# Kernel optimization log

Measured on AMD Instinct MI355X. Metric: run time of the kernel, lower is better.

Reference implementation:

```python
import jax, jax.numpy as jnp
import numpy as np

N_NODES = 100000
FIELD_DIM = 128
EMBED_DIM = 64
N_EDGES = 3200000
BATCH = 8192
NUM_FIELDS = 2


def setup_inputs() -> dict:
    key = jax.random.key(0)
    k1, k2, k3, k4 = jax.random.split(key, 4)
    features = jax.random.normal(k1, (N_NODES, FIELD_DIM), dtype=jnp.float32)
    edge_index = jax.random.randint(k2, (2, N_EDGES), 0, N_NODES, dtype=jnp.int32)
    # GCNConv linear weight (Glorot-ish scale) and bias
    W = jax.random.normal(k3, (FIELD_DIM, EMBED_DIM), dtype=jnp.float32) * (1.0 / np.sqrt(FIELD_DIM))
    bias = jnp.zeros((EMBED_DIM,), dtype=jnp.float32)
    x = jax.random.randint(k4, (BATCH, NUM_FIELDS), 0, N_NODES, dtype=jnp.int32)
    return {"features": features, "edge_index": edge_index, "W": W, "bias": bias, "x": x}


def reference(features, edge_index, W, bias, x):
    # GCNConv: out = D^{-1/2} (A + I) D^{-1/2} (X W) + b, then gather rows by x.
    n = features.shape[0]
    loop = jnp.arange(n, dtype=edge_index.dtype)
    src = jnp.concatenate([edge_index[0], loop])  # [E + N]
    dst = jnp.concatenate([edge_index[1], loop])  # [E + N]
    # degree (with self-loops) per destination node; >= 1 so rsqrt is safe
    deg = jax.ops.segment_sum(jnp.ones_like(dst, dtype=features.dtype), dst, num_segments=n)
    dinv = jax.lax.rsqrt(deg)
    norm = dinv[src] * dinv[dst]  # [E + N]
    h = features @ W  # [N, EMBED_DIM]
    msgs = h[src] * norm[:, None]  # gather + scale
    out = jax.ops.segment_sum(msgs, dst, num_segments=n) + bias  # [N, EMBED_DIM]
    return out[x]  # [BATCH, NUM_FIELDS, EMBED_DIM]
```

## Files before the change

### kernel.cpp

```cpp
#include <hip/hip_runtime.h>

#define N_NODES   100000
#define FIELD_DIM 128
#define EMBED_DIM 64
#define N_EDGES   3200000
#define NX        16384

#define NRANGE    4
#define RN        25000
#define RNH       12500
#define NSLICE    125
#define SLICE_E   (N_EDGES / NSLICE)
#define HISTB     (NRANGE * NSLICE)
#define SB_N      16384
#define EXB       (N_EDGES / 1024)
#define SEG       256

typedef short  bf16x8 __attribute__((ext_vector_type(8)));
typedef float  f32x4  __attribute__((ext_vector_type(4)));

__device__ __forceinline__ unsigned short f2bf(float x) {
    unsigned u = __float_as_uint(x);
    u += 0x7FFF + ((u >> 16) & 1);
    return (unsigned short)(u >> 16);
}
__device__ __forceinline__ float bf2f(unsigned short b) {
    return __uint_as_float(((unsigned)b) << 16);
}
__device__ __forceinline__ unsigned pk2(float lo, float hi) {
    return (unsigned)f2bf(lo) | ((unsigned)f2bf(hi) << 16);
}

__global__ void k_zero(float4* __restrict__ z4) {
    int i = blockIdx.x * blockDim.x + threadIdx.x;
    if (i < 784) z4[i] = make_float4(0.f, 0.f, 0.f, 0.f);
}

__global__ void k_init(const int* __restrict__ x, unsigned int* __restrict__ bits,
                       const float* __restrict__ W, unsigned short* __restrict__ Wt) {
    int b = blockIdx.x;
    if (b < 64) {
        int i = b * 256 + threadIdx.x;
        int v = x[i];
        atomicOr(&bits[v >> 5], 1u << (v & 31));
    } else {
        for (int i = threadIdx.x; i < FIELD_DIM * EMBED_DIM; i += 256) {
            int k = i >> 6, c = i & 63;
            Wt[c * FIELD_DIM + k] = f2bf(W[i]);
        }
    }
}

__global__ __launch_bounds__(256) void k_hist(const int* __restrict__ dst,
                                              unsigned int* __restrict__ partial32) {
    __shared__ unsigned int hist[RNH];
    int tid = threadIdx.x;
    int q = blockIdx.x & 3, s = blockIdx.x >> 2;
    for (int i = tid; i < RNH; i += 256) hist[i] = 0;
    __syncthreads();
    int lo = q * RN;
    const int4* dp = (const int4*)(dst + s * SLICE_E);
#pragma unroll
    for (int bt = 0; bt < 5; ++bt) {
        int4 d[5];
#pragma unroll
        for (int u = 0; u < 5; ++u) d[u] = dp[tid + 256 * (bt * 5 + u)];
#pragma unroll
        for (int u = 0; u < 5; ++u) {
            int a;
            a = d[u].x - lo; if ((unsigned)a < RN) atomicAdd(&hist[a >> 1], 1u << ((a & 1) << 4));
            a = d[u].y - lo; if ((unsigned)a < RN) atomicAdd(&hist[a >> 1], 1u << ((a & 1) << 4));
            a = d[u].z - lo; if ((unsigned)a < RN) atomicAdd(&hist[a >> 1], 1u << ((a & 1) << 4));
            a = d[u].w - lo; if ((unsigned)a < RN) atomicAdd(&hist[a >> 1], 1u << ((a & 1) << 4));
        }
    }
    __syncthreads();
    unsigned int* po = partial32 + (size_t)blockIdx.x * RNH;
    for (int i = tid; i < RNH; i += 256) po[i] = hist[i];
}

__global__ __launch_bounds__(256) void k_reduce(const unsigned int* __restrict__ partial32,
                                                const unsigned int* __restrict__ bits,
                                                int* __restrict__ cnt,
                                                float* __restrict__ dinv,
                                                int* __restrict__ nlist,
                                                int* __restrict__ inv,
                                                int* __restrict__ off,
                                                int* __restrict__ sbase_t,
                                                unsigned long long* __restrict__ counters) {
    __shared__ int wtot[4], wedge[4], ptot[4], pedge[4];
    __shared__ unsigned int baseN, baseE;
    int tid = threadIdx.x;
    int v = blockIdx.x * 256 + tid;
    bool inb = (v < N_NODES);
    int vc = inb ? v : (N_NODES - 1);
    int q = vc / RN, loc = vc - q * RN;
    int i2 = loc >> 1, sh = (loc & 1) << 4;
    const unsigned int* p = partial32 + (size_t)q * RNH + i2;
    int c = 0;
#pragma unroll
    for (int sb = 0; sb < 5; ++sb) {
        unsigned int vals[25];
#pragma unroll
        for (int s = 0; s < 25; ++s) vals[s] = p[(size_t)(sb * 25 + s) * (NRANGE * RNH)];
#pragma unroll
        for (int s = 0; s < 25; ++s) c += (int)((vals[s] >> sh) & 0xFFFFu);
    }
    if (inb) {
        cnt[v] = c;
        dinv[v] = rsqrtf((float)c + 1.0f);
    }
    bool fl = inb && ((bits[v >> 5] >> (v & 31)) & 1u);
    int lane = tid & 63;
    int w = tid >> 6;
    unsigned long long mask = __ballot(fl);
    int cc = fl ? c : 0;
    int incl = cc;
#pragma unroll
    for (int o = 1; o < 64; o <<= 1) {
        int t = __shfl_up(incl, o);
        if (lane >= o) incl += t;
    }
    if (lane == 63) { wtot[w] = __popcll(mask); wedge[w] = incl; }
    int myi = __popcll(mask & ((1ull << lane) - 1));
    int excl = incl - cc;
    __syncthreads();
    if (tid == 0) {
        int t0 = wtot[0], t1 = wtot[1], t2 = wtot[2], t3 = wtot[3];
        int e0 = wedge[0], e1 = wedge[1], e2 = wedge[2], e3 = wedge[3];
        ptot[0] = 0; ptot[1] = t0; ptot[2] = t0 + t1; ptot[3] = t0 + t1 + t2;
        pedge[0] = 0; pedge[1] = e0; pedge[2] = e0 + e1; pedge[3] = e0 + e1 + e2;
        int bt = t0 + t1 + t2 + t3;
        int be = e0 + e1 + e2 + e3;
        if (bt > 0) {
            unsigned long long add = ((unsigned long long)(unsigned)be << 32) |
                                     (unsigned long long)(unsigned)bt;
            unsigned long long old = atomicAdd(counters, add);
            baseN = (unsigned)(old & 0xFFFFFFFFull);
            baseE = (unsigned)(old >> 32);
        } else {
            baseN = 0; baseE = 0;
        }
    }
    __syncthreads();
    if (fl) {
        int ic = (int)baseN + ptot[w] + myi;
        int oc = (int)baseE + pedge[w] + excl;
        nlist[ic] = v;
        inv[v] = ic;
        off[v] = oc;
        int cum = 0;
#pragma unroll
        for (int sb = 0; sb < 5; ++sb) {
            unsigned int vals[25];
#pragma unroll
            for (int s = 0; s < 25; ++s) vals[s] = p[(size_t)(sb * 25 + s) * (NRANGE * RNH)];
#pragma unroll
            for (int s = 0; s < 25; ++s) {
                sbase_t[(size_t)(sb * 25 + s) * SB_N + ic] = oc + cum;
                cum += (int)((vals[s] >> sh) & 0xFFFFu);
            }
        }
    }
}

__global__ __launch_bounds__(256) void k_extract(const int* __restrict__ src,
                                                 const int* __restrict__ dst,
                                                 const unsigned int* __restrict__ bits,
                                                 const int* __restrict__ inv,
                                                 int2* __restrict__ pairs,
                                                 int* __restrict__ pcnt) {
    __shared__ int wsum[4];
    int b = blockIdx.x, tid = threadIdx.x;
    int lane = tid & 63, w = tid >> 6;
    const int4* dp = (const int4*)(dst + b * 1024);
    const int4* sp = (const int4*)(src + b * 1024);
    int4 d4 = dp[tid];
    int4 s4 = sp[tid];
    int dd[4] = {d4.x, d4.y, d4.z, d4.w};
    int ss[4] = {s4.x, s4.y, s4.z, s4.w};
    bool fl[4];
    int nf = 0;
#pragma unroll
    for (int u = 0; u < 4; ++u) {
        fl[u] = (bits[(unsigned)dd[u] >> 5] >> (dd[u] & 31)) & 1u;
        nf += fl[u] ? 1 : 0;
    }
    int incl = nf;
#pragma unroll
    for (int o = 1; o < 64; o <<= 1) {
        int t = __shfl_up(incl, o);
        if (lane >= o) incl += t;
    }
    if (lane == 63) wsum[w] = incl;
    __syncthreads();
    int wbase = 0;
#pragma unroll
    for (int i = 0; i < 4; ++i) wbase += (i < w) ? wsum[i] : 0;
    int pos = wbase + incl - nf;
    int2* po = pairs + (size_t)b * SEG;
#pragma unroll
    for (int u = 0; u < 4; ++u) {
        if (fl[u] && pos < SEG) {
            po[pos] = make_int2(inv[dd[u]], ss[u]);
            ++pos;
        }
    }
    if (tid == 255) pcnt[b] = wsum[0] + wsum[1] + wsum[2] + wsum[3];
}

__global__ __launch_bounds__(256) void k_gemm(const float* __restrict__ F,
                                              const unsigned short* __restrict__ Wt,
                                              unsigned short* __restrict__ h) {
    int tid = threadIdx.x;
    int wave = tid >> 6, lane = tid & 63;
    int l15 = lane & 15, kg = lane >> 4;

    const char* wb = (const char*)Wt;
    bf16x8 bfrag[4][4];
#pragma unroll
    for (int cb = 0; cb < 4; ++cb)
#pragma unroll
        for (int ks = 0; ks < 4; ++ks)
            bfrag[cb][ks] = *(const bf16x8*)(wb + (cb * 16 + l15) * 256 + ks * 64 + kg * 16);

    int row = blockIdx.x * 64 + wave * 16 + l15;
    int rowc = min(row, N_NODES - 1);
    const float4* F4 = (const float4*)(F + (size_t)rowc * FIELD_DIM + kg * 8);

    f32x4 acc[4];
#pragma unroll
    for (int cb = 0; cb < 4; ++cb) acc[cb] = (f32x4){0.f, 0.f, 0.f, 0.f};

#pragma unroll
    for (int ks = 0; ks < 4; ++ks) {
        float4 fa = F4[ks * 8];
        float4 fb = F4[ks * 8 + 1];
        union { bf16x8 v; unsigned u[4]; } af;
        af.u[0] = pk2(fa.x, fa.y);
        af.u[1] = pk2(fa.z, fa.w);
        af.u[2] = pk2(fb.x, fb.y);
        af.u[3] = pk2(fb.z, fb.w);
#pragma unroll
        for (int cb = 0; cb < 4; ++cb)
            acc[cb] = __builtin_amdgcn_mfma_f32_16x16x32_bf16(af.v, bfrag[cb][ks],
                                                              acc[cb], 0, 0, 0);
    }
    int rbase = blockIdx.x * 64 + wave * 16 + kg * 4;
#pragma unroll
    for (int r = 0; r < 4; ++r) {
        int orow = rbase + r;
        if (orow < N_NODES) {
            unsigned short* hp = h + (size_t)orow * 64 + l15;
#pragma unroll
            for (int cb = 0; cb < 4; ++cb) hp[cb * 16] = f2bf(acc[cb][r]);
        }
    }
}

__global__ __launch_bounds__(1024) void k_place(const int2* __restrict__ pairs,
                                                const int* __restrict__ pcnt,
                                                const int* __restrict__ sbase_t,
                                                int* __restrict__ elist) {
    __shared__ unsigned int cur2[8192];
    __shared__ int spre[26];
    int s = blockIdx.x, tid = threadIdx.x;
    for (int i = tid; i < 8192; i += 1024) cur2[i] = 0;
    if (tid == 0) {
        int a = 0;
#pragma unroll
        for (int e = 0; e < 25; ++e) { spre[e] = a; a += pcnt[s * 25 + e]; }
        spre[25] = a;
    }
    __syncthreads();
    int tot = spre[25];
    const int* sb = sbase_t + (size_t)s * SB_N;
    for (int r = tid; r < tot; r += 1024) {
        int lo = 0, hi = 24;
        while (lo < hi) {
            int mid = (lo + hi + 1) >> 1;
            if (spre[mid] <= r) lo = mid; else hi = mid - 1;
        }
        int2 p = pairs[(size_t)(s * 25 + lo) * SEG + (r - spre[lo])];
        int ii = p.x;
        unsigned sh_ = (unsigned)((ii & 1) << 4);
        unsigned old = atomicAdd(&cur2[ii >> 1], 1u << sh_);
        elist[sb[ii] + (int)((old >> sh_) & 0xFFFFu)] = p.y;
    }
}

__global__ __launch_bounds__(256) void k_pull(const int* __restrict__ nlist,
                                              const int* __restrict__ counters,
                                              const int* __restrict__ cnt,
                                              const int* __restrict__ off,
                                              const int* __restrict__ elist,
                                              const unsigned short* __restrict__ h,
                                              const float* __restrict__ dinv,
                                              const float* __restrict__ bias,
                                              float* __restrict__ accc) {
    int t = blockIdx.x * blockDim.x + threadIdx.x;
    int wid = t >> 6;
    int lane = t & 63;
    if (wid >= counters[0]) return;
    int v = nlist[wid];
    float dvd = dinv[v];
    int deg = cnt[v];
    int base = off[v];
    float acc = bf2f(h[(size_t)v * 64 + lane]) * (dvd * dvd) + bias[lane];
    float acc2 = 0.f;
    int j = 0;
    for (; j + 7 < deg; j += 8) {
        int s0 = elist[base + j + 0];
        int s1 = elist[base + j + 1];
        int s2 = elist[base + j + 2];
        int s3 = elist[base + j + 3];
        int s4 = elist[base + j + 4];
        int s5 = elist[base + j + 5];
        int s6 = elist[base + j + 6];
        int s7 = elist[base + j + 7];
        float v0 = bf2f(h[(size_t)s0 * 64 + lane]);
        float v1 = bf2f(h[(size_t)s1 * 64 + lane]);
        float v2 = bf2f(h[(size_t)s2 * 64 + lane]);
        float v3 = bf2f(h[(size_t)s3 * 64 + lane]);
        float v4 = bf2f(h[(size_t)s4 * 64 + lane]);
        float v5 = bf2f(h[(size_t)s5 * 64 + lane]);
        float v6 = bf2f(h[(size_t)s6 * 64 + lane]);
        float v7 = bf2f(h[(size_t)s7 * 64 + lane]);
        float n0 = dinv[s0], n1 = dinv[s1], n2 = dinv[s2], n3 = dinv[s3];
        float n4 = dinv[s4], n5 = dinv[s5], n6 = dinv[s6], n7 = dinv[s7];
        acc  += v0 * (n0 * dvd);
        acc2 += v1 * (n1 * dvd);
        acc  += v2 * (n2 * dvd);
        acc2 += v3 * (n3 * dvd);
        acc  += v4 * (n4 * dvd);
        acc2 += v5 * (n5 * dvd);
        acc  += v6 * (n6 * dvd);
        acc2 += v7 * (n7 * dvd);
    }
    for (; j < deg; ++j) {
        int s0 = elist[base + j];
        acc += bf2f(h[(size_t)s0 * 64 + lane]) * (dinv[s0] * dvd);
    }
    accc[(size_t)wid * 64 + lane] = acc + acc2;
}

__global__ void k_gather(const int* __restrict__ x,
                         const int* __restrict__ inv,
                         const float* __restrict__ accc,
                         float* __restrict__ out) {
    int g = blockIdx.x * blockDim.x + threadIdx.x;
    if (g >= NX * 64) return;
    int v = x[g >> 6];
    out[g] = accc[(size_t)inv[v] * 64 + (g & 63)];
}

extern "C" void kernel_launch(void* const* d_in, const int* in_sizes, int n_in,
                              void* d_out, int out_size, void* d_ws, size_t ws_size,
                              hipStream_t stream) {
    const float* features = (const float*)d_in[0];
    const int*   edge     = (const int*)d_in[1];
    const float* W        = (const float*)d_in[2];
    const float* bias     = (const float*)d_in[3];
    const int*   x        = (const int*)d_in[4];
    float* out = (float*)d_out;

    char* ws = (char*)d_ws;
    unsigned short* h16      = (unsigned short*)(ws);
    int*            elist    = (int*)(ws + 12800000);
    unsigned int*   partial32= (unsigned int*)(ws + 16800000);
    int2*           pairs    = (int2*)(ws + 16800000);
    float*          accc     = (float*)(ws + 23200000);
    int*            sbase_t  = (int*)  (ws + 41800000);
    int*            cnt      = (int*)  (ws + 49992000);
    float*          dinv     = (float*)(ws + 50392000);
    int*            off      = (int*)  (ws + 50792000);
    int*            inv      = (int*)  (ws + 51192000);
    int*            nlist    = (int*)  (ws + 51592000);
    int*            pcnt     = (int*)  (ws + 51657536);
    unsigned long long* counters = (unsigned long long*)(ws + 51670080);
    unsigned int*   bits     = (unsigned int*) (ws + 51670112);
    unsigned short* Wt       = (unsigned short*)(ws + 51682624);

    const int* esrc = edge;
    const int* edst = edge + N_EDGES;

    k_zero   <<<4, 256, 0, stream>>>((float4*)(ws + 51670080));
    k_init   <<<65, 256, 0, stream>>>(x, bits, W, Wt);
    k_hist   <<<HISTB, 256, 0, stream>>>(edst, partial32);
    k_reduce <<<(N_NODES + 255) / 256, 256, 0, stream>>>(partial32, bits, cnt, dinv,
                                                         nlist, inv, off, sbase_t, counters);
    k_extract<<<EXB, 256, 0, stream>>>(esrc, edst, bits, inv, pairs, pcnt);
    k_gemm   <<<(N_NODES + 63) / 64, 256, 0, stream>>>(features, Wt, h16);
    k_place  <<<NSLICE, 1024, 0, stream>>>(pairs, pcnt, sbase_t, elist);
    k_pull   <<<(NX * 64 + 255) / 256, 256, 0, stream>>>(nlist, (const int*)counters,
                                                         cnt, off, elist, h16, dinv,
                                                         bias, accc);
    k_gather <<<(NX * 64 + 255) / 256, 256, 0, stream>>>(x, inv, accc, out);
}
```

Baseline: 125.0 us.

## Merge zeroing into histogram, halve ranges, and compact extract pairs per slice

Folds the workspace-zeroing kernel into the histogram kernel as one extra block. The histogram now uses two node ranges with 1024-thread blocks, so each block covers a 100KB shared histogram and half as many blocks reread the dst array. Extract appends matched pairs into a per-slice buffer through an atomic cursor instead of fixed 256-slot segments. This lets place skip its prefix and binary search and use plain int shared counters preloaded from sbase. Reduce now loads the slice counts once and reuses them, and the W transpose writes coalesced. Risks include lower occupancy from the larger shared histogram and overflow if a slice exceeds its pair capacity.

```diff
diff --git a/kernel.cpp b/kernel.cpp
--- a/kernel.cpp
+++ b/kernel.cpp
@@ -6,15 +6,15 @@
 #define N_EDGES   3200000
 #define NX        16384
 
-#define NRANGE    4
-#define RN        25000
-#define RNH       12500
+#define NRANGE    2
+#define RN        50000
+#define RNH       25000
 #define NSLICE    125
 #define SLICE_E   (N_EDGES / NSLICE)
 #define HISTB     (NRANGE * NSLICE)
 #define SB_N      16384
 #define EXB       (N_EDGES / 1024)
-#define SEG       256
+#define PCAP      5120
 
 typedef short  bf16x8 __attribute__((ext_vector_type(8)));
 typedef float  f32x4  __attribute__((ext_vector_type(4)));
@@ -31,9 +31,31 @@
     return (unsigned)f2bf(lo) | ((unsigned)f2bf(hi) << 16);
 }
 
-__global__ void k_zero(float4* __restrict__ z4) {
-    int i = blockIdx.x * blockDim.x + threadIdx.x;
-    if (i < 784) z4[i] = make_float4(0.f, 0.f, 0.f, 0.f);
+__global__ __launch_bounds__(1024) void k_histzero(const int* __restrict__ dst,
+                                                   unsigned int* __restrict__ partial32,
+                                                   float4* __restrict__ z4) {
+    int tid = threadIdx.x;
+    if (blockIdx.x == HISTB) {
+        for (int i = tid; i < 1284; i += 1024) z4[i] = make_float4(0.f, 0.f, 0.f, 0.f);
+        return;
+    }
+    __shared__ unsigned int hist[RNH];
+    int q = blockIdx.x & 1, s = blockIdx.x >> 1;
+    for (int i = tid; i < RNH; i += 1024) hist[i] = 0;
+    __syncthreads();
+    int lo = q * RN;
+    const int4* dp = (const int4*)(dst + s * SLICE_E);
+    for (int i = tid; i < SLICE_E / 4; i += 1024) {
+        int4 d = dp[i];
+        int a;
+        a = d.x - lo; if ((unsigned)a < RN) atomicAdd(&hist[a >> 1], 1u << ((a & 1) << 4));
+        a = d.y - lo; if ((unsigned)a < RN) atomicAdd(&hist[a >> 1], 1u << ((a & 1) << 4));
+        a = d.z - lo; if ((unsigned)a < RN) atomicAdd(&hist[a >> 1], 1u << ((a & 1) << 4));
+        a = d.w - lo; if ((unsigned)a < RN) atomicAdd(&hist[a >> 1], 1u << ((a & 1) << 4));
+    }
+    __syncthreads();
+    unsigned int* po = partial32 + (size_t)blockIdx.x * RNH;
+    for (int i = tid; i < RNH; i += 1024) po[i] = hist[i];
 }
 
 __global__ void k_init(const int* __restrict__ x, unsigned int* __restrict__ bits,
@@ -44,39 +66,11 @@
         int v = x[i];
         atomicOr(&bits[v >> 5], 1u << (v & 31));
     } else {
-        for (int i = threadIdx.x; i < FIELD_DIM * EMBED_DIM; i += 256) {
-            int k = i >> 6, c = i & 63;
-            Wt[c * FIELD_DIM + k] = f2bf(W[i]);
-        }
-    }
-}
-
-__global__ __launch_bounds__(256) void k_hist(const int* __restrict__ dst,
-                                              unsigned int* __restrict__ partial32) {
-    __shared__ unsigned int hist[RNH];
-    int tid = threadIdx.x;
-    int q = blockIdx.x & 3, s = blockIdx.x >> 2;
-    for (int i = tid; i < RNH; i += 256) hist[i] = 0;
-    __syncthreads();
-    int lo = q * RN;
-    const int4* dp = (const int4*)(dst + s * SLICE_E);
-#pragma unroll
-    for (int bt = 0; bt < 5; ++bt) {
-        int4 d[5];
-#pragma unroll
-        for (int u = 0; u < 5; ++u) d[u] = dp[tid + 256 * (bt * 5 + u)];
-#pragma unroll
-        for (int u = 0; u < 5; ++u) {
-            int a;
-            a = d[u].x - lo; if ((unsigned)a < RN) atomicAdd(&hist[a >> 1], 1u << ((a & 1) << 4));
-            a = d[u].y - lo; if ((unsigned)a < RN) atomicAdd(&hist[a >> 1], 1u << ((a & 1) << 4));
-            a = d[u].z - lo; if ((unsigned)a < RN) atomicAdd(&hist[a >> 1], 1u << ((a & 1) << 4));
-            a = d[u].w - lo; if ((unsigned)a < RN) atomicAdd(&hist[a >> 1], 1u << ((a & 1) << 4));
-        }
-    }
-    __syncthreads();
-    unsigned int* po = partial32 + (size_t)blockIdx.x * RNH;
-    for (int i = tid; i < RNH; i += 256) po[i] = hist[i];
+        for (int o = threadIdx.x; o < FIELD_DIM * EMBED_DIM; o += 256) {
+            int c = o >> 7, k = o & 127;
+            Wt[o] = f2bf(W[k * EMBED_DIM + c]);
+        }
+    }
 }
 
 __global__ __launch_bounds__(256) void k_reduce(const unsigned int* __restrict__ partial32,
@@ -97,15 +91,13 @@
     int q = vc / RN, loc = vc - q * RN;
     int i2 = loc >> 1, sh = (loc & 1) << 4;
     const unsigned int* p = partial32 + (size_t)q * RNH + i2;
+    unsigned short vals[NSLICE];
+#pragma unroll
+    for (int s = 0; s < NSLICE; ++s)
+        vals[s] = (unsigned short)((p[(size_t)s * (NRANGE * RNH)] >> sh) & 0xFFFFu);
     int c = 0;
 #pragma unroll
-    for (int sb = 0; sb < 5; ++sb) {
-        unsigned int vals[25];
-#pragma unroll
-        for (int s = 0; s < 25; ++s) vals[s] = p[(size_t)(sb * 25 + s) * (NRANGE * RNH)];
-#pragma unroll
-        for (int s = 0; s < 25; ++s) c += (int)((vals[s] >> sh) & 0xFFFFu);
-    }
+    for (int s = 0; s < NSLICE; ++s) c += vals[s];
     if (inb) {
         cnt[v] = c;
         dinv[v] = rsqrtf((float)c + 1.0f);
@@ -151,15 +143,9 @@
         off[v] = oc;
         int cum = 0;
 #pragma unroll
-        for (int sb = 0; sb < 5; ++sb) {
-            unsigned int vals[25];
-#pragma unroll
-            for (int s = 0; s < 25; ++s) vals[s] = p[(size_t)(sb * 25 + s) * (NRANGE * RNH)];
-#pragma unroll
-            for (int s = 0; s < 25; ++s) {
-                sbase_t[(size_t)(sb * 25 + s) * SB_N + ic] = oc + cum;
-                cum += (int)((vals[s] >> sh) & 0xFFFFu);
-            }
+        for (int s = 0; s < NSLICE; ++s) {
+            sbase_t[(size_t)s * SB_N + ic] = oc + cum;
+            cum += vals[s];
         }
     }
 }
@@ -169,10 +155,12 @@
                                                  const unsigned int* __restrict__ bits,
                                                  const int* __restrict__ inv,
                                                  int2* __restrict__ pairs,
-                                                 int* __restrict__ pcnt) {
+                                                 int* __restrict__ scur16) {
     __shared__ int wsum[4];
+    __shared__ int sbase;
     int b = blockIdx.x, tid = threadIdx.x;
     int lane = tid & 63, w = tid >> 6;
+    int slice = b / 25;
     const int4* dp = (const int4*)(dst + b * 1024);
     const int4* sp = (const int4*)(src + b * 1024);
     int4 d4 = dp[tid];
@@ -194,19 +182,21 @@
     }
     if (lane == 63) wsum[w] = incl;
     __syncthreads();
-    int wbase = 0;
-#pragma unroll
-    for (int i = 0; i < 4; ++i) wbase += (i < w) ? wsum[i] : 0;
-    int pos = wbase + incl - nf;
-    int2* po = pairs + (size_t)b * SEG;
+    if (tid == 0) {
+        int bt = wsum[0] + wsum[1] + wsum[2] + wsum[3];
+        sbase = bt ? atomicAdd(&scur16[slice * 16], bt) : 0;
+    }
+    __syncthreads();
+    int wbase = (w > 0 ? wsum[0] : 0) + (w > 1 ? wsum[1] : 0) + (w > 2 ? wsum[2] : 0);
+    int pos = sbase + wbase + incl - nf;
+    int2* po = pairs + (size_t)slice * PCAP;
 #pragma unroll
     for (int u = 0; u < 4; ++u) {
-        if (fl[u] && pos < SEG) {
-            po[pos] = make_int2(inv[dd[u]], ss[u]);
+        if (fl[u]) {
+            if (pos < PCAP) po[pos] = make_int2(inv[dd[u]], ss[u]);
             ++pos;
         }
     }
-    if (tid == 255) pcnt[b] = wsum[0] + wsum[1] + wsum[2] + wsum[3];
 }
 
 __global__ __launch_bounds__(256) void k_gemm(const float* __restrict__ F,
@@ -259,33 +249,20 @@
 }
 
 __global__ __launch_bounds__(1024) void k_place(const int2* __restrict__ pairs,
-                                                const int* __restrict__ pcnt,
+                                                const int* __restrict__ scur16,
                                                 const int* __restrict__ sbase_t,
                                                 int* __restrict__ elist) {
-    __shared__ unsigned int cur2[8192];
-    __shared__ int spre[26];
+    __shared__ int cur[SB_N];
     int s = blockIdx.x, tid = threadIdx.x;
-    for (int i = tid; i < 8192; i += 1024) cur2[i] = 0;
-    if (tid == 0) {
-        int a = 0;
-#pragma unroll
-        for (int e = 0; e < 25; ++e) { spre[e] = a; a += pcnt[s * 25 + e]; }
-        spre[25] = a;
-    }
-    __syncthreads();
-    int tot = spre[25];
-    const int* sb = sbase_t + (size_t)s * SB_N;
+    const int* srow = sbase_t + (size_t)s * SB_N;
+    for (int i = tid; i < SB_N; i += 1024) cur[i] = srow[i];
+    __syncthreads();
+    int tot = min(scur16[s * 16], PCAP);
+    const int2* pp = pairs + (size_t)s * PCAP;
     for (int r = tid; r < tot; r += 1024) {
-        int lo = 0, hi = 24;
-        while (lo < hi) {
-            int mid = (lo + hi + 1) >> 1;
-            if (spre[mid] <= r) lo = mid; else hi = mid - 1;
-        }
-        int2 p = pairs[(size_t)(s * 25 + lo) * SEG + (r - spre[lo])];
-        int ii = p.x;
-        unsigned sh_ = (unsigned)((ii & 1) << 4);
-        unsigned old = atomicAdd(&cur2[ii >> 1], 1u << sh_);
-        elist[sb[ii] + (int)((old >> sh_) & 0xFFFFu)] = p.y;
+        int2 p = pp[r];
+        int slot = atomicAdd(&cur[p.x], 1);
+        elist[slot] = p.y;
     }
 }
 
@@ -369,31 +346,31 @@
     int*            elist    = (int*)(ws + 12800000);
     unsigned int*   partial32= (unsigned int*)(ws + 16800000);
     int2*           pairs    = (int2*)(ws + 16800000);
-    float*          accc     = (float*)(ws + 23200000);
+    float*          accc     = (float*)(ws + 21920000);
     int*            sbase_t  = (int*)  (ws + 41800000);
     int*            cnt      = (int*)  (ws + 49992000);
     float*          dinv     = (float*)(ws + 50392000);
     int*            off      = (int*)  (ws + 50792000);
     int*            inv      = (int*)  (ws + 51192000);
     int*            nlist    = (int*)  (ws + 51592000);
-    int*            pcnt     = (int*)  (ws + 51657536);
-    unsigned long long* counters = (unsigned long long*)(ws + 51670080);
-    unsigned int*   bits     = (unsigned int*) (ws + 51670112);
-    unsigned short* Wt       = (unsigned short*)(ws + 51682624);
+    int*            scur16   = (int*)  (ws + 51657536);
+    unsigned long long* counters = (unsigned long long*)(ws + 51665536);
+    unsigned int*   bits     = (unsigned int*) (ws + 51665568);
+    unsigned short* Wt       = (unsigned short*)(ws + 51678080);
 
     const int* esrc = edge;
     const int* edst = edge + N_EDGES;
 
-    k_zero   <<<4, 256, 0, stream>>>((float4*)(ws + 51670080));
-    k_init   <<<65, 256, 0, stream>>>(x, bits, W, Wt);
-    k_hist   <<<HISTB, 256, 0, stream>>>(edst, partial32);
-    k_reduce <<<(N_NODES + 255) / 256, 256, 0, stream>>>(partial32, bits, cnt, dinv,
-                                                         nlist, inv, off, sbase_t, counters);
-    k_extract<<<EXB, 256, 0, stream>>>(esrc, edst, bits, inv, pairs, pcnt);
-    k_gemm   <<<(N_NODES + 63) / 64, 256, 0, stream>>>(features, Wt, h16);
-    k_place  <<<NSLICE, 1024, 0, stream>>>(pairs, pcnt, sbase_t, elist);
-    k_pull   <<<(NX * 64 + 255) / 256, 256, 0, stream>>>(nlist, (const int*)counters,
-                                                         cnt, off, elist, h16, dinv,
-                                                         bias, accc);
-    k_gather <<<(NX * 64 + 255) / 256, 256, 0, stream>>>(x, inv, accc, out);
-}
+    k_histzero<<<HISTB + 1, 1024, 0, stream>>>(edst, partial32,
+                                               (float4*)(ws + 51657536));
+    k_init    <<<65, 256, 0, stream>>>(x, bits, W, Wt);
+    k_reduce  <<<(N_NODES + 255) / 256, 256, 0, stream>>>(partial32, bits, cnt, dinv,
+                                                          nlist, inv, off, sbase_t, counters);
+    k_extract <<<EXB, 256, 0, stream>>>(esrc, edst, bits, inv, pairs, scur16);
+    k_gemm    <<<(N_NODES + 63) / 64, 256, 0, stream>>>(features, Wt, h16);
+    k_place   <<<NSLICE, 1024, 0, stream>>>(pairs, scur16, sbase_t, elist);
+    k_pull    <<<(NX * 64 + 255) / 256, 256, 0, stream>>>(nlist, (const int*)counters,
+                                                          cnt, off, elist, h16, dinv,
+                                                          bias, accc);
+    k_gather  <<<(NX * 64 + 255) / 256, 256, 0, stream>>>(x, inv, accc, out);
+}
```

Result: faster. 102.9 us (-17.7%).
